# Kernel tuning notes

Hardware: AMD Instinct MI355X
Metric: run time of the kernel (lower is better)

The kernel has to match this reference:

```python
import jax, jax.numpy as jnp
import numpy as np

D = 1024
H = 16
DH = D // H
MAX_TYPES = 256
B, L = 8, 1024
EPS = 1e-5


def setup_inputs() -> dict:
    key = jax.random.key(0)
    ks = jax.random.split(key, 16)
    s = 0.02
    return {
        'type_ids': jax.random.randint(ks[0], (B, L), 0, MAX_TYPES),
        'values': jax.random.normal(ks[1], (B, L, 1), jnp.float32),
        'deltas': jax.random.uniform(ks[2], (B, L, 1), jnp.float32),
        'type_emb': jax.random.normal(ks[3], (MAX_TYPES, D), jnp.float32) * s,
        'Wv': jax.random.normal(ks[4], (D, 1), jnp.float32) * s,
        'bv': jnp.zeros((D,), jnp.float32),
        'Wt': jax.random.normal(ks[5], (D, 1), jnp.float32) * s,
        'bt': jnp.zeros((D,), jnp.float32),
        'Win': jax.random.normal(ks[6], (3 * D, D), jnp.float32) * s,
        'bin': jnp.zeros((3 * D,), jnp.float32),
        'Wout': jax.random.normal(ks[7], (D, D), jnp.float32) * s,
        'bout': jnp.zeros((D,), jnp.float32),
        'W1': jax.random.normal(ks[8], (D, D), jnp.float32) * s,
        'b1': jnp.zeros((D,), jnp.float32),
        'W2': jax.random.normal(ks[9], (D, D), jnp.float32) * s,
        'b2': jnp.zeros((D,), jnp.float32),
        'gamma': jnp.ones((D,), jnp.float32),
        'beta': jnp.zeros((D,), jnp.float32),
    }


def _ln(x, gamma, beta):
    mu = jnp.mean(x, axis=-1, keepdims=True)
    var = jnp.mean(jnp.square(x - mu), axis=-1, keepdims=True)
    return (x - mu) * jax.lax.rsqrt(var + EPS) * gamma + beta


def reference(type_ids, values, deltas, type_emb, Wv, bv, Wt, bt,
              Win, bin, Wout, bout, W1, b1, W2, b2, gamma, beta):
    # fused embedding: type lookup + value/time linear projections
    h = type_emb[type_ids] + values @ Wv.T + bv + deltas @ Wt.T + bt  # [B,L,D]
    b, l, d = h.shape
    # multi-head self-attention (explicit weights path, need_weights=True)
    qkv = h @ Win.T + bin  # [B,L,3D]
    q, k, v = jnp.split(qkv, 3, axis=-1)
    q = q.reshape(b, l, H, DH)
    k = k.reshape(b, l, H, DH)
    v = v.reshape(b, l, H, DH)
    scale = 1.0 / jnp.sqrt(jnp.asarray(DH, h.dtype))
    scores = jnp.einsum('blhd,bmhd->bhlm', q, k) * scale  # [B,H,L,L]
    w = jax.nn.softmax(scores, axis=-1)
    attn = jnp.einsum('bhlm,bmhd->blhd', w, v).reshape(b, l, d)
    attn_out = attn @ Wout.T + bout
    h2 = _ln(h + attn_out, gamma, beta)
    ff = jax.nn.relu(h2 @ W1.T + b1) @ W2.T + b2
    h3 = _ln(h2 + ff, gamma, beta)
    pooled = h3.mean(axis=1)  # [B,D]
    attn_tokens = w.mean(axis=1).mean(axis=2)  # mean over heads, then keys -> [B,L]
    return pooled, attn_tokens
```

## Files before the change

kernel.cpp:

```cpp
#include <hip/hip_runtime.h>
#include <hip/hip_bf16.h>


#define Dm 1024
#define Hh 16
#define Bb 8
#define Ll 1024
#define Mm 8192
#define LNEPS 1e-5f
#define QSCALE 0.18033688f

typedef __attribute__((ext_vector_type(8))) short s16x8;
typedef __attribute__((ext_vector_type(4))) short s16x4;
typedef __attribute__((ext_vector_type(4))) float f32x4;

using bf16 = __hip_bfloat16;

__device__ __forceinline__ short f2bs(float f) {
  return __builtin_bit_cast(short, __float2bfloat16(f));
}
__device__ __forceinline__ float b2f(short s) {
  return __builtin_bit_cast(float, ((unsigned)(unsigned short)s) << 16);
}

__device__ __forceinline__ unsigned cvtpk(float lo, float hi) {
  unsigned r;
  asm("v_cvt_pk_bf16_f32 %0, %1, %2" : "=v"(r) : "v"(lo), "v"(hi));
  return r;
}

__device__ __forceinline__ void gload16(const void* g, void* l) {
  __builtin_amdgcn_global_load_lds(
      (__attribute__((address_space(1))) void*)g,
      (__attribute__((address_space(3))) void*)l, 16, 0, 0);
}

__global__ __launch_bounds__(256) void k_prep(
    const float* __restrict__ w0, const float* __restrict__ w1,
    const float* __restrict__ w2, const float* __restrict__ w3,
    bf16* __restrict__ o0, bf16* __restrict__ o1,
    bf16* __restrict__ o2, bf16* __restrict__ o3,
    const int* __restrict__ tids, const float* __restrict__ vals,
    const float* __restrict__ dels, const float* __restrict__ temb,
    const float* __restrict__ Wv, const float* __restrict__ bv,
    const float* __restrict__ Wt, const float* __restrict__ bt,
    bf16* __restrict__ hb)
{
  const int bId = blockIdx.x;
  if (bId < 6144) {
    const float* src; bf16* dst; int rel;
    float sc = 1.f;
    if (bId < 3072)      { src = w0; dst = o0; rel = bId; if (bId < 1024) sc = QSCALE; }
    else if (bId < 4096) { src = w1; dst = o1; rel = bId - 3072; }
    else if (bId < 5120) { src = w2; dst = o2; rel = bId - 4096; }
    else                 { src = w3; dst = o3; rel = bId - 5120; }
    const size_t i = ((size_t)rel * 256 + threadIdx.x) * 4;
    const float4 v = *(const float4*)&src[i];
    s16x4 o;
    o[0] = f2bs(v.x * sc); o[1] = f2bs(v.y * sc); o[2] = f2bs(v.z * sc); o[3] = f2bs(v.w * sc);
    *(s16x4*)&dst[i] = o;
  } else {
    const int row = bId - 6144;
    const int ty = tids[row];
    const float v = vals[row], dl = dels[row];
    const int d0 = threadIdx.x * 4;
    const float4 e  = *(const float4*)&temb[(size_t)ty * Dm + d0];
    const float4 wv = *(const float4*)&Wv[d0];
    const float4 c1 = *(const float4*)&bv[d0];
    const float4 wt = *(const float4*)&Wt[d0];
    const float4 c2 = *(const float4*)&bt[d0];
    s16x4 o;
    o[0] = f2bs(e.x + v * wv.x + c1.x + dl * wt.x + c2.x);
    o[1] = f2bs(e.y + v * wv.y + c1.y + dl * wt.y + c2.y);
    o[2] = f2bs(e.z + v * wv.z + c1.z + dl * wt.z + c2.z);
    o[3] = f2bs(e.w + v * wv.w + c1.w + dl * wt.w + c2.w);
    *(s16x4*)((short*)hb + (size_t)row * Dm + d0) = o;
  }
}

template<bool RELU, bool RES, bool QS, bool VT>
__global__ __launch_bounds__(512) void k_gemm8(
    const bf16* __restrict__ A, const bf16* __restrict__ Bt,
    const float* __restrict__ bias, const bf16* __restrict__ res,
    bf16* __restrict__ outB, bf16* __restrict__ vt, const int N, const int K)
{
  __shared__ __attribute__((aligned(16))) short lds[49152];
  const int tid = threadIdx.x, lane = tid & 63, wave = tid >> 6;
  const int wr = wave >> 2, wc = wave & 3;
  const int l15 = lane & 15, lg = (lane >> 4) & 3;
  const int bm = blockIdx.x, bn = blockIdx.y;
  const int NT = K >> 6;

  const int rl = tid >> 3;
  const int swz = ((tid & 7) ^ (rl & 7)) * 8;
  const bf16* aSrc = A  + (size_t)(bm * 128 + rl) * K + swz;
  const bf16* bSrc = Bt + (size_t)(bn * 256 + rl) * K + swz;

  f32x4 acc[4][4] = {};

  auto stageA = [&](int t, int h) {
    gload16(aSrc + (size_t)h * 64 * K + t * 64,
            &lds[(t & 1) * 24576 + h * 4096 + tid * 8]);
  };
  auto stageB = [&](int t, int h) {
    gload16(bSrc + (size_t)h * 128 * K + t * 64,
            &lds[(t & 1) * 24576 + 8192 + h * 8192 + tid * 8]);
    gload16(bSrc + (size_t)(h * 128 + 64) * K + t * 64,
            &lds[(t & 1) * 24576 + 8192 + h * 8192 + 4096 + tid * 8]);
  };

  stageA(0, 0); stageA(0, 1); stageB(0, 0); stageB(0, 1);
  if (NT > 1) { stageA(1, 0); stageA(1, 1); }
  asm volatile("s_waitcnt vmcnt(2)" ::: "memory");
  __builtin_amdgcn_sched_barrier(0);
  __builtin_amdgcn_s_barrier();

  for (int t = 0; t < NT; ++t) {
    const int cb = (t & 1) * 24576;
    s16x8 fa[4][2], fb[2][2];

#pragma unroll
    for (int m = 0; m < 4; ++m)
#pragma unroll
      for (int ks = 0; ks < 2; ++ks) {
        const int row = wr * 64 + m * 16 + l15;
        fa[m][ks] = *(const s16x8*)&lds[cb + row * 64 + (((ks * 4 + lg) ^ (row & 7)) << 3)];
      }
#pragma unroll
    for (int n = 0; n < 2; ++n)
#pragma unroll
      for (int ks = 0; ks < 2; ++ks) {
        const int row = wc * 64 + n * 16 + l15;
        fb[n][ks] = *(const s16x8*)&lds[cb + 8192 + row * 64 + (((ks * 4 + lg) ^ (row & 7)) << 3)];
      }
    if (t + 1 < NT) { stageB(t + 1, 0); stageB(t + 1, 1); }
    __builtin_amdgcn_s_barrier();
    asm volatile("s_waitcnt lgkmcnt(0)" ::: "memory");
    __builtin_amdgcn_sched_barrier(0);
    __builtin_amdgcn_s_setprio(1);
#pragma unroll
    for (int m = 0; m < 4; ++m)
#pragma unroll
      for (int n = 0; n < 2; ++n)
#pragma unroll
        for (int ks = 0; ks < 2; ++ks)
          acc[m][n] = __builtin_amdgcn_mfma_f32_16x16x32_bf16(fa[m][ks], fb[n][ks], acc[m][n], 0, 0, 0);
    __builtin_amdgcn_s_setprio(0);
    __builtin_amdgcn_s_barrier();

#pragma unroll
    for (int n = 0; n < 2; ++n)
#pragma unroll
      for (int ks = 0; ks < 2; ++ks) {
        const int row = wc * 64 + (2 + n) * 16 + l15;
        fb[n][ks] = *(const s16x8*)&lds[cb + 8192 + row * 64 + (((ks * 4 + lg) ^ (row & 7)) << 3)];
      }
    if (t + 2 < NT) { stageA(t + 2, 0); stageA(t + 2, 1); }
    __builtin_amdgcn_s_barrier();
    asm volatile("s_waitcnt lgkmcnt(0)" ::: "memory");
    __builtin_amdgcn_sched_barrier(0);
    __builtin_amdgcn_s_setprio(1);
#pragma unroll
    for (int m = 0; m < 4; ++m)
#pragma unroll
      for (int n = 0; n < 2; ++n)
#pragma unroll
        for (int ks = 0; ks < 2; ++ks)
          acc[m][2 + n] = __builtin_amdgcn_mfma_f32_16x16x32_bf16(fa[m][ks], fb[n][ks], acc[m][2 + n], 0, 0, 0);
    __builtin_amdgcn_s_setprio(0);

    if (t + 1 < NT) {
      if (t + 2 < NT) asm volatile("s_waitcnt vmcnt(2)" ::: "memory");
      else            asm volatile("s_waitcnt vmcnt(0)" ::: "memory");
      __builtin_amdgcn_sched_barrier(0);
      __builtin_amdgcn_s_barrier();
    }
  }

#pragma unroll
  for (int n = 0; n < 4; ++n) {
    const int col = bn * 256 + wc * 64 + n * 16 + l15;
    float bc = bias[col];
    if constexpr (QS) { if (col < 1024) bc *= QSCALE; }
    if constexpr (VT) {
      if (col >= 2048) {
        const int hh = (col - 2048) >> 6, dh = (col - 2048) & 63;
#pragma unroll
        for (int m = 0; m < 4; ++m) {
          const size_t row0 = (size_t)bm * 128 + wr * 64 + m * 16 + lg * 4;
          const int bb = (int)(row0 >> 10), l0 = (int)(row0 & 1023);
          s16x4 pk;
#pragma unroll
          for (int i = 0; i < 4; ++i) pk[i] = f2bs(acc[m][n][i] + bc);
          *(s16x4*)((short*)vt + ((size_t)((bb * 16 + hh) * 64 + dh)) * Ll + l0) = pk;
        }
        continue;
      }
    }
#pragma unroll
    for (int m = 0; m < 4; ++m) {
#pragma unroll
      for (int i = 0; i < 4; ++i) {
        const size_t row = (size_t)bm * 128 + wr * 64 + m * 16 + lg * 4 + i;
        float v = acc[m][n][i] + bc;
        if constexpr (RES)  v += b2f(((const short*)res)[row * N + col]);
        if constexpr (RELU) v = fmaxf(v, 0.f);
        outB[row * N + col] = __float2bfloat16(v);
      }
    }
  }
}

__global__ __launch_bounds__(256) void k_attn(
    const bf16* __restrict__ qkv, const bf16* __restrict__ vt, bf16* __restrict__ attnb)
{
  const int bh = blockIdx.x;
  const int qb = blockIdx.y;
  const int b = bh >> 4, h = bh & 15;
  __shared__ __attribute__((aligned(16))) short lK[8192];
  __shared__ __attribute__((aligned(16))) short lV[8192];
  __shared__ __attribute__((aligned(16))) short lP[8192];
  const int tid = threadIdx.x, lane = tid & 63, wave = tid >> 6;
  const int l15 = lane & 15, lg = lane >> 4;
  const int qrow = wave * 32;
  const int l7 = l15 & 7;

  s16x8 qf[2][2];
#pragma unroll
  for (int mq = 0; mq < 2; ++mq)
#pragma unroll
    for (int ks = 0; ks < 2; ++ks)
      qf[mq][ks] = *(const s16x8*)((const short*)qkv +
          ((size_t)(b * Ll + qb * 128 + qrow + mq * 16 + l15)) * 3072 + h * 64 + ks * 32 + lg * 8);

  f32x4 o[2][4] = {};
  float rs[2] = {0.f, 0.f};

  const int sr = tid >> 3;
  const int swz = (tid & 7) ^ (sr & 7);

  auto stage = [&](int mc) {
    const int bo = (mc & 1) * 4096;
    const bf16* gk = qkv + ((size_t)(b * Ll + mc * 64 + sr)) * 3072 + 1024 + h * 64 + swz * 8;
    gload16(gk,                     &lK[bo + tid * 8]);
    gload16(gk + (size_t)32 * 3072, &lK[bo + 2048 + tid * 8]);
    const bf16* gv = vt + ((size_t)(bh * 64 + sr)) * Ll + mc * 64 + swz * 8;
    gload16(gv,                   &lV[bo + tid * 8]);
    gload16(gv + (size_t)32 * Ll, &lV[bo + 2048 + tid * 8]);
  };

  stage(0);

  for (int mc = 0; mc < 16; ++mc) {
    asm volatile("s_waitcnt vmcnt(0)" ::: "memory");
    __builtin_amdgcn_s_barrier();
    __builtin_amdgcn_sched_barrier(0);
    if (mc + 1 < 16) stage(mc + 1);
    const int bo = (mc & 1) * 4096;

    f32x4 st[2][4] = {};
    __builtin_amdgcn_s_setprio(1);
#pragma unroll
    for (int ks = 0; ks < 2; ++ks) {
#pragma unroll
      for (int n = 0; n < 4; ++n) {
        const int kr = n * 16 + l15;
        const s16x8 kf = *(const s16x8*)&lK[bo + kr * 64 + (((ks * 4 + lg) ^ l7) << 3)];
        st[0][n] = __builtin_amdgcn_mfma_f32_16x16x32_bf16(kf, qf[0][ks], st[0][n], 0, 0, 0);
        st[1][n] = __builtin_amdgcn_mfma_f32_16x16x32_bf16(kf, qf[1][ks], st[1][n], 0, 0, 0);
      }
    }
    __builtin_amdgcn_s_setprio(0);

#pragma unroll
    for (int mq = 0; mq < 2; ++mq) {
      const int qr = qrow + mq * 16 + l15;
      short* prow = &lP[qr * 64];
      float loc = 0.f;
#pragma unroll
      for (int n = 0; n < 4; ++n) {
        const float e0 = __builtin_amdgcn_exp2f(st[mq][n][0]);
        const float e1 = __builtin_amdgcn_exp2f(st[mq][n][1]);
        const float e2 = __builtin_amdgcn_exp2f(st[mq][n][2]);
        const float e3 = __builtin_amdgcn_exp2f(st[mq][n][3]);
        loc += (e0 + e1) + (e2 + e3);
        const unsigned c0 = cvtpk(e0, e1);
        const unsigned c1 = cvtpk(e2, e3);
        const int col0 = n * 16 + lg * 4;
        const int scol = ((((col0 >> 3) ^ (qr & 7)) << 3) | (col0 & 7));
        *(unsigned*)&prow[scol]     = c0;
        *(unsigned*)&prow[scol + 2] = c1;
      }
      rs[mq] += loc;
    }

    __builtin_amdgcn_s_setprio(1);
#pragma unroll
    for (int ks = 0; ks < 2; ++ks) {
      s16x8 pa[2];
#pragma unroll
      for (int mq = 0; mq < 2; ++mq) {
        const int qr = qrow + mq * 16 + l15;
        pa[mq] = *(const s16x8*)&lP[qr * 64 + (((ks * 4 + lg) ^ (qr & 7)) << 3)];
      }
#pragma unroll
      for (int dn = 0; dn < 4; ++dn) {
        const int vr = dn * 16 + l15;
        const s16x8 vf = *(const s16x8*)&lV[bo + vr * 64 + (((ks * 4 + lg) ^ l7) << 3)];
        o[0][dn] = __builtin_amdgcn_mfma_f32_16x16x32_bf16(pa[0], vf, o[0][dn], 0, 0, 0);
        o[1][dn] = __builtin_amdgcn_mfma_f32_16x16x32_bf16(pa[1], vf, o[1][dn], 0, 0, 0);
      }
    }
    __builtin_amdgcn_s_setprio(0);
    asm volatile("s_waitcnt lgkmcnt(0)" ::: "memory");
  }

#pragma unroll
  for (int mq = 0; mq < 2; ++mq) {
    rs[mq] += __shfl_xor(rs[mq], 16);
    rs[mq] += __shfl_xor(rs[mq], 32);
  }
#pragma unroll
  for (int mq = 0; mq < 2; ++mq) {
    float inv[4];
#pragma unroll
    for (int i = 0; i < 4; ++i)
      inv[i] = 1.f / __shfl(rs[mq], lg * 4 + i);
#pragma unroll
    for (int dn = 0; dn < 4; ++dn) {
#pragma unroll
      for (int i = 0; i < 4; ++i) {
        const int q = qb * 128 + qrow + mq * 16 + lg * 4 + i;
        attnb[((size_t)(b * Ll + q)) * Dm + h * 64 + dn * 16 + l15] =
            __float2bfloat16(o[mq][dn][i] * inv[i]);
      }
    }
  }
}

__global__ __launch_bounds__(256) void k_ln(const bf16* __restrict__ x,
    const float* __restrict__ gamma, const float* __restrict__ beta,
    bf16* __restrict__ y)
{
  const size_t row = blockIdx.x;
  const int d0 = threadIdx.x * 4;
  const s16x4 xv = *(const s16x4*)((const short*)x + row * Dm + d0);
  float f0 = b2f(xv[0]), f1 = b2f(xv[1]), f2 = b2f(xv[2]), f3 = b2f(xv[3]);
  float s  = (f0 + f1) + (f2 + f3);
  float ss = (f0 * f0 + f1 * f1) + (f2 * f2 + f3 * f3);
#pragma unroll
  for (int m = 1; m < 64; m <<= 1) { s += __shfl_xor(s, m); ss += __shfl_xor(ss, m); }
  __shared__ float red[8];
  const int wv = threadIdx.x >> 6;
  if ((threadIdx.x & 63) == 0) { red[wv] = s; red[4 + wv] = ss; }
  __syncthreads();
  s  = red[0] + red[1] + red[2] + red[3];
  ss = red[4] + red[5] + red[6] + red[7];
  const float mu = s * (1.f / Dm);
  const float rstd = rsqrtf(ss * (1.f / Dm) - mu * mu + LNEPS);
  const float4 g  = *(const float4*)&gamma[d0];
  const float4 be = *(const float4*)&beta[d0];
  s16x4 o;
  o[0] = f2bs((f0 - mu) * rstd * g.x + be.x);
  o[1] = f2bs((f1 - mu) * rstd * g.y + be.y);
  o[2] = f2bs((f2 - mu) * rstd * g.z + be.z);
  o[3] = f2bs((f3 - mu) * rstd * g.w + be.w);
  *(s16x4*)((short*)y + row * Dm + d0) = o;
}

__global__ __launch_bounds__(256) void k_pool_part(const bf16* __restrict__ h3, float* __restrict__ part)
{
  const int b = blockIdx.x, lcn = blockIdx.y, dz = blockIdx.z;
  const int d = dz * 256 + threadIdx.x;
  float s = 0.f;
#pragma unroll 4
  for (int l = 0; l < 64; ++l)
    s += b2f(((const short*)h3)[((size_t)(b * Ll + lcn * 64 + l)) * Dm + d]);
  part[((size_t)(b * 16 + lcn)) * Dm + d] = s;
}

__global__ __launch_bounds__(256) void k_pool_fin(const float* __restrict__ part, float* __restrict__ out)
{
  const int b = blockIdx.x;
  const int d = blockIdx.y * 256 + threadIdx.x;
  float s = 0.f;
#pragma unroll
  for (int c = 0; c < 16; ++c) s += part[((size_t)(b * 16 + c)) * Dm + d];
  out[b * Dm + d] = s * (1.f / Ll);
  out[(size_t)Mm + b * Dm + d] = 1.f / Ll;
}

extern "C" void kernel_launch(void* const* d_in, const int* in_sizes, int n_in,
                              void* d_out, int out_size, void* d_ws, size_t ws_size,
                              hipStream_t stream) {
  const int*   tids  = (const int*)  d_in[0];
  const float* vals  = (const float*)d_in[1];
  const float* dels  = (const float*)d_in[2];
  const float* temb  = (const float*)d_in[3];
  const float* Wv    = (const float*)d_in[4];
  const float* bv    = (const float*)d_in[5];
  const float* Wt    = (const float*)d_in[6];
  const float* bt    = (const float*)d_in[7];
  const float* Win   = (const float*)d_in[8];
  const float* bin   = (const float*)d_in[9];
  const float* Wout  = (const float*)d_in[10];
  const float* bout  = (const float*)d_in[11];
  const float* W1    = (const float*)d_in[12];
  const float* b1    = (const float*)d_in[13];
  const float* W2    = (const float*)d_in[14];
  const float* b2    = (const float*)d_in[15];
  const float* gamma = (const float*)d_in[16];
  const float* beta  = (const float*)d_in[17];
  float* out = (float*)d_out;

  char* w = (char*)d_ws;
  const size_t MB = 1ull << 20;
  bf16*  hb    = (bf16*) (w + 0);
  bf16*  qkv   = (bf16*) (w + 16 * MB);
  bf16*  vtb   = (bf16*) (w + 64 * MB);
  bf16*  attnb = (bf16*) (w + 80 * MB);
  bf16*  x1b   = (bf16*) (w + 16 * MB);
  bf16*  h2b   = (bf16*) (w + 32 * MB);
  bf16*  ff1   = (bf16*) (w + 48 * MB);
  bf16*  x2b   = (bf16*) (w + 64 * MB);
  bf16*  h3b   = (bf16*) (w + 80 * MB);
  bf16*  WinB  = (bf16*) (w + 96 * MB);
  bf16*  WoutB = (bf16*) (w + 102 * MB);
  bf16*  W1B   = (bf16*) (w + 104 * MB);
  bf16*  W2B   = (bf16*) (w + 106 * MB);
  float* part  = (float*)(w + 108 * MB);

  k_prep<<<14336, 256, 0, stream>>>(Win, Wout, W1, W2, WinB, WoutB, W1B, W2B,
                                    tids, vals, dels, temb, Wv, bv, Wt, bt, hb);

  k_gemm8<false, false, true, true><<<dim3(64, 12), 512, 0, stream>>>(
      hb, WinB, bin, nullptr, qkv, vtb, 3072, 1024);

  k_attn<<<dim3(128, 8), 256, 0, stream>>>(qkv, vtb, attnb);

  k_gemm8<false, true, false, false><<<dim3(64, 4), 512, 0, stream>>>(
      attnb, WoutB, bout, hb, x1b, nullptr, 1024, 1024);

  k_ln<<<Mm, 256, 0, stream>>>(x1b, gamma, beta, h2b);

  k_gemm8<true, false, false, false><<<dim3(64, 4), 512, 0, stream>>>(
      h2b, W1B, b1, nullptr, ff1, nullptr, 1024, 1024);

  k_gemm8<false, true, false, false><<<dim3(64, 4), 512, 0, stream>>>(
      ff1, W2B, b2, h2b, x2b, nullptr, 1024, 1024);

  k_ln<<<Mm, 256, 0, stream>>>(x2b, gamma, beta, h3b);

  k_pool_part<<<dim3(8, 16, 4), 256, 0, stream>>>(h3b, part);
  k_pool_fin<<<dim3(8, 4), 256, 0, stream>>>(part, out);
}
```

Baseline: 230.0 us.

## Use dedicated 256x256-tile GEMM kernel for QKV projection

Adds a dedicated QKV projection kernel that computes 256x256 output tiles per block instead of 128x256, with 8x4 accumulators per wave and a split A/B staging pipeline across two half-K phases using 128 KB of LDS. It halves the grid to 32x12 blocks to raise arithmetic intensity and cut global reloads of A and B for the largest GEMM. The generic GEMM template drops its QS/VT epilogue paths. The cost is doubled accumulator registers, a larger LDS footprint that limits occupancy to one block per CU, and only 384 blocks, which may leave the 256-CU device poorly balanced.

Result: slower. 241.4 us (+5.0%).

```diff
diff --git a/kernel.cpp b/kernel.cpp
--- a/kernel.cpp
+++ b/kernel.cpp
@@ -78,11 +78,135 @@
   }
 }
 
-template<bool RELU, bool RES, bool QS, bool VT>
+__global__ __launch_bounds__(512) void k_gemmQ(
+    const bf16* __restrict__ A, const bf16* __restrict__ Bt,
+    const float* __restrict__ bias,
+    bf16* __restrict__ outB, bf16* __restrict__ vt, const int N, const int K)
+{
+  __shared__ __attribute__((aligned(16))) short lds[65536];
+  const int tid = threadIdx.x, lane = tid & 63, wave = tid >> 6;
+  const int wr = wave >> 2, wc = wave & 3;
+  const int l15 = lane & 15, lg = (lane >> 4) & 3;
+  const int bm = blockIdx.x, bn = blockIdx.y;
+  const int NT = K >> 6;
+
+  const int rl = tid >> 3;
+  const int swz = ((tid & 7) ^ (rl & 7)) * 8;
+  const bf16* aSrc = A  + (size_t)(bm * 256 + rl) * K + swz;
+  const bf16* bSrc = Bt + (size_t)(bn * 256 + rl) * K + swz;
+
+  f32x4 acc[8][4] = {};
+
+  auto stageA = [&](int t) {
+    const int base = (t & 1) * 32768;
+    gload16(aSrc + t * 64,                    &lds[base         + tid * 8]);
+    gload16(aSrc + (size_t) 64 * K + t * 64,  &lds[base +  4096 + tid * 8]);
+    gload16(aSrc + (size_t)128 * K + t * 64,  &lds[base +  8192 + tid * 8]);
+    gload16(aSrc + (size_t)192 * K + t * 64,  &lds[base + 12288 + tid * 8]);
+  };
+  auto stageB = [&](int t) {
+    const int base = (t & 1) * 32768 + 16384;
+    gload16(bSrc + t * 64,                    &lds[base         + tid * 8]);
+    gload16(bSrc + (size_t) 64 * K + t * 64,  &lds[base +  4096 + tid * 8]);
+    gload16(bSrc + (size_t)128 * K + t * 64,  &lds[base +  8192 + tid * 8]);
+    gload16(bSrc + (size_t)192 * K + t * 64,  &lds[base + 12288 + tid * 8]);
+  };
+
+  stageA(0); stageB(0);
+  asm volatile("s_waitcnt vmcnt(0)" ::: "memory");
+  __builtin_amdgcn_sched_barrier(0);
+  __builtin_amdgcn_s_barrier();
+
+  for (int t = 0; t < NT; ++t) {
+    const int cb = (t & 1) * 32768;
+    s16x8 fa[8], fb[4];
+
+#pragma unroll
+    for (int m = 0; m < 8; ++m) {
+      const int row = wr * 128 + m * 16 + l15;
+      fa[m] = *(const s16x8*)&lds[cb + row * 64 + ((lg ^ (row & 7)) << 3)];
+    }
+#pragma unroll
+    for (int n = 0; n < 4; ++n) {
+      const int row = wc * 64 + n * 16 + l15;
+      fb[n] = *(const s16x8*)&lds[cb + 16384 + row * 64 + ((lg ^ (row & 7)) << 3)];
+    }
+    if (t + 1 < NT) stageA(t + 1);
+    __builtin_amdgcn_s_barrier();
+    asm volatile("s_waitcnt lgkmcnt(0)" ::: "memory");
+    __builtin_amdgcn_sched_barrier(0);
+    __builtin_amdgcn_s_setprio(1);
+#pragma unroll
+    for (int m = 0; m < 8; ++m)
+#pragma unroll
+      for (int n = 0; n < 4; ++n)
+        acc[m][n] = __builtin_amdgcn_mfma_f32_16x16x32_bf16(fa[m], fb[n], acc[m][n], 0, 0, 0);
+    __builtin_amdgcn_s_setprio(0);
+    __builtin_amdgcn_s_barrier();
+
+#pragma unroll
+    for (int m = 0; m < 8; ++m) {
+      const int row = wr * 128 + m * 16 + l15;
+      fa[m] = *(const s16x8*)&lds[cb + row * 64 + (((4 + lg) ^ (row & 7)) << 3)];
+    }
+#pragma unroll
+    for (int n = 0; n < 4; ++n) {
+      const int row = wc * 64 + n * 16 + l15;
+      fb[n] = *(const s16x8*)&lds[cb + 16384 + row * 64 + (((4 + lg) ^ (row & 7)) << 3)];
+    }
+    if (t + 1 < NT) stageB(t + 1);
+    __builtin_amdgcn_s_barrier();
+    asm volatile("s_waitcnt lgkmcnt(0)" ::: "memory");
+    __builtin_amdgcn_sched_barrier(0);
+    __builtin_amdgcn_s_setprio(1);
+#pragma unroll
+    for (int m = 0; m < 8; ++m)
+#pragma unroll
+      for (int n = 0; n < 4; ++n)
+        acc[m][n] = __builtin_amdgcn_mfma_f32_16x16x32_bf16(fa[m], fb[n], acc[m][n], 0, 0, 0);
+    __builtin_amdgcn_s_setprio(0);
+
+    if (t + 1 < NT) {
+      asm volatile("s_waitcnt vmcnt(0)" ::: "memory");
+      __builtin_amdgcn_sched_barrier(0);
+      __builtin_amdgcn_s_barrier();
+    }
+  }
+
+#pragma unroll
+  for (int n = 0; n < 4; ++n) {
+    const int col = bn * 256 + wc * 64 + n * 16 + l15;
+    float bc = bias[col];
+    if (col < 1024) bc *= QSCALE;
+    if (col >= 2048) {
+      const int hh = (col - 2048) >> 6, dh = (col - 2048) & 63;
+#pragma unroll
+      for (int m = 0; m < 8; ++m) {
+        const size_t row0 = (size_t)bm * 256 + wr * 128 + m * 16 + lg * 4;
+        const int bb = (int)(row0 >> 10), l0 = (int)(row0 & 1023);
+        s16x4 pk;
+#pragma unroll
+        for (int i = 0; i < 4; ++i) pk[i] = f2bs(acc[m][n][i] + bc);
+        *(s16x4*)((short*)vt + ((size_t)((bb * 16 + hh) * 64 + dh)) * Ll + l0) = pk;
+      }
+    } else {
+#pragma unroll
+      for (int m = 0; m < 8; ++m) {
+#pragma unroll
+        for (int i = 0; i < 4; ++i) {
+          const size_t row = (size_t)bm * 256 + wr * 128 + m * 16 + lg * 4 + i;
+          outB[row * N + col] = __float2bfloat16(acc[m][n][i] + bc);
+        }
+      }
+    }
+  }
+}
+
+template<bool RELU, bool RES>
 __global__ __launch_bounds__(512) void k_gemm8(
     const bf16* __restrict__ A, const bf16* __restrict__ Bt,
     const float* __restrict__ bias, const bf16* __restrict__ res,
-    bf16* __restrict__ outB, bf16* __restrict__ vt, const int N, const int K)
+    bf16* __restrict__ outB, const int N, const int K)
 {
   __shared__ __attribute__((aligned(16))) short lds[49152];
   const int tid = threadIdx.x, lane = tid & 63, wave = tid >> 6;
@@ -180,23 +304,7 @@
 #pragma unroll
   for (int n = 0; n < 4; ++n) {
     const int col = bn * 256 + wc * 64 + n * 16 + l15;
-    float bc = bias[col];
-    if constexpr (QS) { if (col < 1024) bc *= QSCALE; }
-    if constexpr (VT) {
-      if (col >= 2048) {
-        const int hh = (col - 2048) >> 6, dh = (col - 2048) & 63;
-#pragma unroll
-        for (int m = 0; m < 4; ++m) {
-          const size_t row0 = (size_t)bm * 128 + wr * 64 + m * 16 + lg * 4;
-          const int bb = (int)(row0 >> 10), l0 = (int)(row0 & 1023);
-          s16x4 pk;
-#pragma unroll
-          for (int i = 0; i < 4; ++i) pk[i] = f2bs(acc[m][n][i] + bc);
-          *(s16x4*)((short*)vt + ((size_t)((bb * 16 + hh) * 64 + dh)) * Ll + l0) = pk;
-        }
-        continue;
-      }
-    }
+    const float bc = bias[col];
 #pragma unroll
     for (int m = 0; m < 4; ++m) {
 #pragma unroll
@@ -433,21 +541,20 @@
   k_prep<<<14336, 256, 0, stream>>>(Win, Wout, W1, W2, WinB, WoutB, W1B, W2B,
                                     tids, vals, dels, temb, Wv, bv, Wt, bt, hb);
 
-  k_gemm8<false, false, true, true><<<dim3(64, 12), 512, 0, stream>>>(
-      hb, WinB, bin, nullptr, qkv, vtb, 3072, 1024);
+  k_gemmQ<<<dim3(32, 12), 512, 0, stream>>>(hb, WinB, bin, qkv, vtb, 3072, 1024);
 
   k_attn<<<dim3(128, 8), 256, 0, stream>>>(qkv, vtb, attnb);
 
-  k_gemm8<false, true, false, false><<<dim3(64, 4), 512, 0, stream>>>(
-      attnb, WoutB, bout, hb, x1b, nullptr, 1024, 1024);
+  k_gemm8<false, true><<<dim3(64, 4), 512, 0, stream>>>(
+      attnb, WoutB, bout, hb, x1b, 1024, 1024);
 
   k_ln<<<Mm, 256, 0, stream>>>(x1b, gamma, beta, h2b);
 
-  k_gemm8<true, false, false, false><<<dim3(64, 4), 512, 0, stream>>>(
-      h2b, W1B, b1, nullptr, ff1, nullptr, 1024, 1024);
-
-  k_gemm8<false, true, false, false><<<dim3(64, 4), 512, 0, stream>>>(
-      ff1, W2B, b2, h2b, x2b, nullptr, 1024, 1024);
+  k_gemm8<true, false><<<dim3(64, 4), 512, 0, stream>>>(
+      h2b, W1B, b1, nullptr, ff1, 1024, 1024);
+
+  k_gemm8<false, true><<<dim3(64, 4), 512, 0, stream>>>(
+      ff1, W2B, b2, h2b, x2b, 1024, 1024);
 
   k_ln<<<Mm, 256, 0, stream>>>(x2b, gamma, beta, h3b);
 
```
